# Kernel optimization log

Measured on AMD Instinct MI355X. Metric: run time of the kernel, lower is better.

Reference implementation:

```python
import jax, jax.numpy as jnp
import numpy as np
import math

B, NO, L = 128, 100, 36
VS, TS, D, H, NB = 2048, 1024, 1024, 8, 2
DH = D // H
SCALE = 1.0 / math.sqrt(DH)


def _shape(x):
    # [B, N, D] -> [B, H, N, DH]
    b, n, _ = x.shape
    return x.reshape(b, n, H, DH).transpose(0, 2, 1, 3)


def _unshape(x):
    # [B, H, N, DH] -> [B, N, D]
    return x.transpose(0, 2, 1, 3).reshape(x.shape[0], x.shape[2], D)


def _masked_softmax(scores, key_mask):
    # scores [B,H,Nq,Nk]; key_mask [B,Nk] float (1=valid, 0=pad)
    scores = jnp.where(key_mask[:, None, None, :] > 0, scores, -jnp.inf)
    return jax.nn.softmax(scores, axis=-1)


def _forward(v, t, vm, tm,
             vlin_w, vlin_b, tlin_w, tlin_b,
             iv_w, iv_b, it_w, it_b, ivo_w, ivo_b, ito_w, ito_b,
             gv_w, gv_b, gt_w, gt_b, av_w, av_b, at_w, at_b,
             avo_w, avo_b, ato_w, ato_b):
    # initial projection to hidden size (dropout is identity at drop=0.0)
    v = v @ vlin_w + vlin_b
    t = t @ tlin_w + tlin_b
    for _ in range(NB):  # weights shared across blocks (SingleBlock)
        # ---- InterModalityUpdate ----
        v = v * vm[..., None]
        t = t * tm[..., None]
        vt = jax.nn.relu(v) @ iv_w + iv_b   # [B,NO,3D]
        tt = jax.nn.relu(t) @ it_w + it_b   # [B,L,3D]
        vk, vq, vv = [_shape(a) for a in jnp.split(vt, 3, axis=2)]
        tk, tq, tv = [_shape(a) for a in jnp.split(tt, 3, axis=2)]
        t2v = _masked_softmax(jnp.einsum('bhnd,bhmd->bhnm', vq, tk) * SCALE, tm)
        v2t = _masked_softmax(jnp.einsum('bhnd,bhmd->bhnm', tq, vk) * SCALE, vm)
        v_up = _unshape(jnp.einsum('bhnm,bhmd->bhnd', t2v, tv))
        t_up = _unshape(jnp.einsum('bhnm,bhmd->bhnd', v2t, vv))
        v = jnp.concatenate([v, v_up], axis=2) @ ivo_w + ivo_b
        t = jnp.concatenate([t, t_up], axis=2) @ ito_w + ito_b
        # ---- DyIntraModalityUpdate ----
        v_mean = (v * vm[..., None]).sum(1) / vm.sum(1, keepdims=True)  # [B,D]
        t_mean = (t * tm[..., None]).sum(1) / tm.sum(1, keepdims=True)
        v4t_gate = jax.nn.sigmoid(jax.nn.relu(v_mean) @ gv_w + gv_b)  # gates text
        t4v_gate = jax.nn.sigmoid(jax.nn.relu(t_mean) @ gt_w + gt_b)  # gates vision
        gate_t = (1.0 + v4t_gate).reshape(-1, H, 1, DH)  # [B,H,1,DH]
        gate_v = (1.0 + t4v_gate).reshape(-1, H, 1, DH)
        vt2 = (jax.nn.relu(v) @ av_w + av_b) * vm[..., None]
        tt2 = (jax.nn.relu(t) @ at_w + at_b) * tm[..., None]
        vk2, vq2, vv2 = [_shape(a) for a in jnp.split(vt2, 3, axis=2)]
        tk2, tq2, tv2 = [_shape(a) for a in jnp.split(tt2, 3, axis=2)]
        v2v = _masked_softmax(jnp.einsum('bhnd,bhmd->bhnm', gate_v * vq2, gate_v * vk2) * SCALE, vm)
        t2t = _masked_softmax(jnp.einsum('bhnd,bhmd->bhnm', gate_t * tq2, gate_t * tk2) * SCALE, tm)
        v_up2 = _unshape(jnp.einsum('bhnm,bhmd->bhnd', v2v, vv2))
        t_up2 = _unshape(jnp.einsum('bhnm,bhmd->bhnd', t2t, tv2))
        v = (v + v_up2) @ avo_w + avo_b
        t = (t + t_up2) @ ato_w + ato_b
    return v, t


def setup_inputs() -> dict:
    key = jax.random.key(0)
    ks = list(jax.random.split(key, 20))
    WS = 0.02  # weight init scale

    def rn(k, shape, s=1.0):
        return jax.random.normal(k, shape, dtype=jnp.float32) * s

    inp = {
        'v': rn(ks[0], (B, NO, VS)),
        't': rn(ks[1], (B, L, TS)),
        'v_mask': jnp.ones((B, NO), dtype=jnp.float32),
        't_mask': jnp.ones((B, L), dtype=jnp.float32),
        'vlin_w': rn(ks[2], (VS, D), WS), 'vlin_b': jnp.zeros((D,), jnp.float32),
        'tlin_w': rn(ks[3], (TS, D), WS), 'tlin_b': jnp.zeros((D,), jnp.float32),
        'iv_w': rn(ks[4], (D, 3 * D), WS), 'iv_b': jnp.zeros((3 * D,), jnp.float32),
        'it_w': rn(ks[5], (D, 3 * D), WS), 'it_b': jnp.zeros((3 * D,), jnp.float32),
        'ivo_w': rn(ks[6], (2 * D, D), WS), 'ivo_b': jnp.zeros((D,), jnp.float32),
        'ito_w': rn(ks[7], (2 * D, D), WS), 'ito_b': jnp.zeros((D,), jnp.float32),
        'gv_w': rn(ks[8], (D, D), WS), 'gv_b': jnp.zeros((D,), jnp.float32),
        'gt_w': rn(ks[9], (D, D), WS), 'gt_b': jnp.zeros((D,), jnp.float32),
        'av_w': rn(ks[10], (D, 3 * D), WS), 'av_b': jnp.zeros((3 * D,), jnp.float32),
        'at_w': rn(ks[11], (D, 3 * D), WS), 'at_b': jnp.zeros((3 * D,), jnp.float32),
        'avo_w': rn(ks[12], (D, D), WS), 'avo_b': jnp.zeros((D,), jnp.float32),
        'ato_w': rn(ks[13], (D, D), WS), 'ato_b': jnp.zeros((D,), jnp.float32),
    }
    return inp


def reference(v, t, v_mask, t_mask,
              vlin_w, vlin_b, tlin_w, tlin_b,
              iv_w, iv_b, it_w, it_b, ivo_w, ivo_b, ito_w, ito_b,
              gv_w, gv_b, gt_w, gt_b, av_w, av_b, at_w, at_b,
              avo_w, avo_b, ato_w, ato_b):
    return _forward(v, t, v_mask, t_mask,
                    vlin_w, vlin_b, tlin_w, tlin_b,
                    iv_w, iv_b, it_w, it_b, ivo_w, ivo_b, ito_w, ito_b,
                    gv_w, gv_b, gt_w, gt_b, av_w, av_b, at_w, at_b,
                    avo_w, avo_b, ato_w, ato_b)
```

## Files before the change

### kernel.cpp

```cpp
#include <hip/hip_runtime.h>

typedef __bf16 bf16x8 __attribute__((ext_vector_type(8)));
typedef float f32x4 __attribute__((ext_vector_type(4)));

#define SCALEF 0.08838834764831843f
#define FL_SIG 2

__device__ __forceinline__ float bf2f(short u) {
    unsigned int x = ((unsigned int)(unsigned short)u) << 16;
    return __builtin_bit_cast(float, x);
}
__device__ __forceinline__ short f2bf(float f) {
    unsigned int x = __builtin_bit_cast(unsigned int, f);
    unsigned int r = (x + 0x7FFFu + ((x >> 16) & 1u)) >> 16;
    return (short)(unsigned short)r;
}
__device__ __forceinline__ unsigned int pkbf(float lo, float hi) {
    return ((unsigned int)(unsigned short)f2bf(lo)) | (((unsigned int)(unsigned short)f2bf(hi)) << 16);
}
__device__ __forceinline__ unsigned int relu_pk(unsigned int p) {
    unsigned int sgn = p & 0x80008000u;
    unsigned int m = (sgn >> 15) * 0xFFFFu;
    return p & ~m;
}
__device__ __forceinline__ void gload16(const void* g, void* l) {
    __builtin_amdgcn_global_load_lds(
        (const __attribute__((address_space(1))) unsigned int*)g,
        (__attribute__((address_space(3))) unsigned int*)l, 16, 0, 0);
}

struct GP {
    const short* A1; const short* A2; const short* WT;
    const float* bias; const float* rmask; void* C;
    int k2s, lda, M, N, K, ldc, flags;
};

template<int RELU, int CF32>
__global__ __launch_bounds__(256, 4) void gemm2_k(GP p0, GP p1)
{
    GP p = (blockIdx.z == 0) ? p0 : p1;
    const int nbx = p.N >> 7;
    const int nby = p.M >> 7;
    if ((int)blockIdx.y >= nby) return;

    __shared__ short lA[128 * 64];
    __shared__ short lB[128 * 64];
    const int tid = threadIdx.x;
    const int lane = tid & 63;
    const int wave = tid >> 6;
    const int wr = wave >> 1, wc = wave & 1;
    const int q16 = lane & 15, gk = lane >> 4;

    const int nwg = nbx * nby;
    int orig = blockIdx.y * nbx + blockIdx.x;
    int qq = nwg >> 3, rr = nwg & 7;
    int xcd = orig & 7, idx = orig >> 3;
    int swz = (xcd < rr ? xcd * (qq + 1) : rr * (qq + 1) + (xcd - rr) * qq) + idx;
    const int bn = (swz % nbx) * 128;
    const int bm = (swz / nbx) * 128;

    const int srow = lane >> 3;
    const int scol = ((lane & 7) ^ srow) * 8;

    f32x4 acc[4][4];
#pragma unroll
    for (int i = 0; i < 4; ++i)
#pragma unroll
        for (int j = 0; j < 4; ++j) acc[i][j] = (f32x4){0.f, 0.f, 0.f, 0.f};

    for (int k0 = 0; k0 < p.K; k0 += 64) {
        const short* Asrc = p.A1; int kc = k0;
        if (p.A2 != nullptr && k0 >= p.k2s) { Asrc = p.A2; kc = k0 - p.k2s; }
#pragma unroll
        for (int i = 0; i < 4; ++i) {
            int chunk = wave * 4 + i;
            int row = chunk * 8 + srow;
            gload16(Asrc + (size_t)(bm + row) * p.lda + kc + scol, lA + chunk * 512);
            gload16(p.WT + (size_t)(bn + row) * p.K + k0 + scol, lB + chunk * 512);
        }
        __syncthreads();
#pragma unroll
        for (int kk = 0; kk < 2; ++kk) {
            bf16x8 af[4], bfr[4];
#pragma unroll
            for (int i = 0; i < 4; ++i) {
                int row = wr * 64 + i * 16 + q16;
                int off = (row * 128 + kk * 64 + gk * 16) ^ ((row & 7) << 4);
                af[i] = *(const bf16x8*)((const char*)lA + off);
                if (RELU) {
                    union { bf16x8 v; unsigned int w[4]; } u;
                    u.v = af[i];
#pragma unroll
                    for (int t = 0; t < 4; ++t) u.w[t] = relu_pk(u.w[t]);
                    af[i] = u.v;
                }
            }
#pragma unroll
            for (int j = 0; j < 4; ++j) {
                int row = wc * 64 + j * 16 + q16;
                int off = (row * 128 + kk * 64 + gk * 16) ^ ((row & 7) << 4);
                bfr[j] = *(const bf16x8*)((const char*)lB + off);
            }
#pragma unroll
            for (int i = 0; i < 4; ++i)
#pragma unroll
                for (int j = 0; j < 4; ++j)
                    acc[i][j] = __builtin_amdgcn_mfma_f32_16x16x32_bf16(af[i], bfr[j], acc[i][j], 0, 0, 0);
        }
        __syncthreads();
    }
    const bool sig = (p.flags & FL_SIG) != 0;
#pragma unroll
    for (int i = 0; i < 4; ++i) {
#pragma unroll
        for (int j = 0; j < 4; ++j) {
            int col = bn + wc * 64 + j * 16 + q16;
            float bv = p.bias[col];
#pragma unroll
            for (int r = 0; r < 4; ++r) {
                int row = bm + wr * 64 + i * 16 + gk * 4 + r;
                float v = acc[i][j][r] + bv;
                if (sig) v = 1.f + 1.f / (1.f + __expf(-v));
                if (p.rmask) v *= p.rmask[row];
                if (CF32) ((float*)p.C)[(size_t)row * p.ldc + col] = v;
                else      ((short*)p.C)[(size_t)row * p.ldc + col] = f2bf(v);
            }
        }
    }
}

struct AP {
    const short* q; const short* kv; const float* mask; const short* gate;
    const short* add; short* out; int Nq, Nk;
};

__global__ __launch_bounds__(256, 2) void attn2_mfma(AP a0, AP a1)
{
    constexpr int KT = 7, KT2 = 4;
    constexpr int KROWS = KT * 16;
    constexpr int KV = KT2 * 32;
    constexpr int VROWB = KV * 2;
    __shared__ short sK[KROWS * 128];
    __shared__ short sVT[128 * KV];
    __shared__ float sMask[KV];

    AP a = (blockIdx.z == 0) ? a0 : a1;
    const int Nq = a.Nq, Nk = a.Nk;
    const int tid = threadIdx.x;
    const int h = blockIdx.x, b = blockIdx.y;
    const int lane = tid & 63, w = tid >> 6;
    const int g = lane >> 4, q16 = lane & 15;

    union U8 { uint4 u4; short s[8]; };

    for (int u = tid; u < Nk * 16; u += 256) {
        int k = u >> 4, seg = u & 15;
        U8 t; t.u4 = *(const uint4*)(a.kv + (size_t)(b * Nk + k) * 3072 + h * 128 + seg * 8);
        if (a.gate) {
            const short* gp = a.gate + b * 1024 + h * 128 + seg * 8;
#pragma unroll
            for (int j = 0; j < 8; ++j) {
                float gv = bf2f(gp[j]);
                t.s[j] = f2bf(bf2f(t.s[j]) * gv * gv);
            }
        }
        int off = (k * 256 + seg * 16) ^ ((k & 7) << 4);
        *(uint4*)((char*)sK + off) = t.u4;
    }
    for (int u = tid; u < Nk * 16; u += 256) {
        int k = u >> 4, seg = u & 15;
        U8 t; t.u4 = *(const uint4*)(a.kv + (size_t)(b * Nk + k) * 3072 + 2048 + h * 128 + seg * 8);
#pragma unroll
        for (int j = 0; j < 8; ++j) {
            int d = seg * 8 + j;
            int off = (d * VROWB + ((k >> 3) << 4) + (k & 7) * 2) ^ ((d & 7) << 4);
            *(short*)((char*)sVT + off) = t.s[j];
        }
    }
    for (int u = tid; u < (KV - Nk) * 128; u += 256) {
        int k = Nk + (u >> 7), d = u & 127;
        int off = (d * VROWB + ((k >> 3) << 4) + (k & 7) * 2) ^ ((d & 7) << 4);
        *(short*)((char*)sVT + off) = 0;
    }
    for (int u = tid; u < KV; u += 256)
        sMask[u] = (u < Nk) ? a.mask[b * Nk + u] : 0.f;
    __syncthreads();

    const int QT = (Nq + 15) >> 4;
    for (int qt = w; qt < QT; qt += 4) {
        int qrow = qt * 16 + q16; if (qrow >= Nq) qrow = Nq - 1;
        const short* qp = a.q + (size_t)(b * Nq + qrow) * 3072 + 1024 + h * 128 + g * 8;
        bf16x8 qf[4];
#pragma unroll
        for (int ks = 0; ks < 4; ++ks)
            qf[ks] = *(const bf16x8*)(qp + ks * 32);

        f32x4 accs[KT];
#pragma unroll
        for (int kt = 0; kt < KT; ++kt) accs[kt] = (f32x4){0.f, 0.f, 0.f, 0.f};
#pragma unroll
        for (int kt = 0; kt < KT; ++kt) {
            int krow = kt * 16 + q16;
#pragma unroll
            for (int ks = 0; ks < 4; ++ks) {
                bf16x8 kf = *(const bf16x8*)((char*)sK +
                    ((krow * 256 + ks * 64 + g * 16) ^ ((krow & 7) << 4)));
                accs[kt] = __builtin_amdgcn_mfma_f32_16x16x32_bf16(kf, qf[ks], accs[kt], 0, 0, 0);
            }
        }
        float pv[KT][4];
        float mx = -__builtin_inff();
#pragma unroll
        for (int kt = 0; kt < KT; ++kt)
#pragma unroll
            for (int r = 0; r < 4; ++r) {
                int k = kt * 16 + g * 4 + r;
                float s = (sMask[k] > 0.f) ? accs[kt][r] * SCALEF : -__builtin_inff();
                pv[kt][r] = s;
                mx = fmaxf(mx, s);
            }
        mx = fmaxf(mx, __shfl_xor(mx, 16, 64));
        mx = fmaxf(mx, __shfl_xor(mx, 32, 64));
        float sum = 0.f;
#pragma unroll
        for (int kt = 0; kt < KT; ++kt)
#pragma unroll
            for (int r = 0; r < 4; ++r) {
                float p = __expf(pv[kt][r] - mx);
                pv[kt][r] = p;
                sum += p;
            }
        sum += __shfl_xor(sum, 16, 64);
        sum += __shfl_xor(sum, 32, 64);
        float rden = 1.f / sum;

        unsigned int wA[KT2 * 2], wB[KT2 * 2];
#pragma unroll
        for (int t = 0; t < KT2 * 2; ++t) {
            if (t < KT) { wA[t] = pkbf(pv[t][0], pv[t][1]); wB[t] = pkbf(pv[t][2], pv[t][3]); }
            else { wA[t] = 0u; wB[t] = 0u; }
        }
        f32x4 acco[8];
#pragma unroll
        for (int dt = 0; dt < 8; ++dt) acco[dt] = (f32x4){0.f, 0.f, 0.f, 0.f};
        const int srcA = (((g & 1) * 2) * 16 + q16) * 4;
        const int srcB = (((g & 1) * 2 + 1) * 16 + q16) * 4;
        const bool hi = g >= 2;
#pragma unroll
        for (int kt2 = 0; kt2 < KT2; ++kt2) {
            int a0_ = __builtin_amdgcn_ds_bpermute(srcA, (int)wA[2 * kt2]);
            int a1_ = __builtin_amdgcn_ds_bpermute(srcA, (int)wA[2 * kt2 + 1]);
            int b0_ = __builtin_amdgcn_ds_bpermute(srcA, (int)wB[2 * kt2]);
            int b1_ = __builtin_amdgcn_ds_bpermute(srcA, (int)wB[2 * kt2 + 1]);
            int c0_ = __builtin_amdgcn_ds_bpermute(srcB, (int)wA[2 * kt2]);
            int c1_ = __builtin_amdgcn_ds_bpermute(srcB, (int)wA[2 * kt2 + 1]);
            int d0_ = __builtin_amdgcn_ds_bpermute(srcB, (int)wB[2 * kt2]);
            int d1_ = __builtin_amdgcn_ds_bpermute(srcB, (int)wB[2 * kt2 + 1]);
            union { int wd[4]; bf16x8 v; } pf;
            pf.wd[0] = hi ? a1_ : a0_;
            pf.wd[1] = hi ? b1_ : b0_;
            pf.wd[2] = hi ? c1_ : c0_;
            pf.wd[3] = hi ? d1_ : d0_;
#pragma unroll
            for (int dt = 0; dt < 8; ++dt) {
                int drow = dt * 16 + q16;
                bf16x8 vf = *(const bf16x8*)((char*)sVT +
                    ((drow * VROWB + kt2 * 64 + g * 16) ^ ((drow & 7) << 4)));
                acco[dt] = __builtin_amdgcn_mfma_f32_16x16x32_bf16(pf.v, vf, acco[dt], 0, 0, 0);
            }
        }
        float rd[4];
#pragma unroll
        for (int r = 0; r < 4; ++r) {
            int rv = __builtin_amdgcn_ds_bpermute((g * 4 + r) * 4, __builtin_bit_cast(int, rden));
            rd[r] = __builtin_bit_cast(float, rv);
        }
#pragma unroll
        for (int dt = 0; dt < 8; ++dt)
#pragma unroll
            for (int r = 0; r < 4; ++r) {
                int q = qt * 16 + g * 4 + r;
                if (q < Nq) {
                    size_t oidx = (size_t)(b * Nq + q) * 1024 + h * 128 + dt * 16 + q16;
                    float val = acco[dt][r] * rd[r];
                    if (a.add) val += bf2f(a.add[oidx]);
                    a.out[oidx] = f2bf(val);
                }
            }
    }
}

struct TP { const float* W; short* WT; int K, N, nblk; };
struct TPack { TP t[12]; };

__global__ void transpose12_k(TPack pk) {
    __shared__ short tile[32][33];
    int bid = blockIdx.x;
    int pi = 0;
    while (bid >= pk.t[pi].nblk) { bid -= pk.t[pi].nblk; ++pi; }
    const float* W = pk.t[pi].W;
    short* WT = pk.t[pi].WT;
    int K = pk.t[pi].K, N = pk.t[pi].N;
    int nbx = N >> 5;
    int nb = (bid % nbx) * 32, kb = (bid / nbx) * 32;
    int tx = threadIdx.x & 31, ty = threadIdx.x >> 5;
    for (int i = ty; i < 32; i += 8)
        tile[i][tx] = f2bf(W[(size_t)(kb + i) * N + nb + tx]);
    __syncthreads();
    for (int i = ty; i < 32; i += 8)
        WT[(size_t)(nb + i) * K + kb + tx] = tile[tx][i];
}

__global__ void cvt2_bf(const float* __restrict__ a, short* __restrict__ oa, int na8,
                        const float* __restrict__ b, short* __restrict__ ob, int nb8) {
    int i = blockIdx.x * 256 + threadIdx.x;
    const float* src; short* dst; int loc;
    if (i < na8) { src = a; dst = oa; loc = i; }
    else if (i < na8 + nb8) { src = b; dst = ob; loc = i - na8; }
    else return;
    const float4* p = (const float4*)(src + (size_t)loc * 8);
    float4 x = p[0], y = p[1];
    uint4 val;
    val.x = pkbf(x.x, x.y); val.y = pkbf(x.z, x.w);
    val.z = pkbf(y.x, y.y); val.w = pkbf(y.z, y.w);
    *(uint4*)(dst + (size_t)loc * 8) = val;
}

__global__ void mean2_k(const short* __restrict__ Xv, const float* __restrict__ mv, short* __restrict__ ov_,
                        const short* __restrict__ Xt, const float* __restrict__ mt, short* __restrict__ ot_) {
    int idx = blockIdx.x * 256 + threadIdx.x;
    const short* X; const float* mk; short* o; int N; int loc;
    if (idx < 131072) { X = Xv; mk = mv; o = ov_; N = 100; loc = idx; }
    else { X = Xt; mk = mt; o = ot_; N = 36; loc = idx - 131072; }
    int b = loc >> 10, d = loc & 1023;
    float s = 0.f, c = 0.f;
    for (int n = 0; n < N; ++n) {
        float m = mk[b * N + n];
        s += bf2f(X[(size_t)(b * N + n) * 1024 + d]) * m;
        c += m;
    }
    o[loc] = f2bf(s / c);
}

extern "C" void kernel_launch(void* const* d_in, const int* in_sizes, int n_in,
                              void* d_out, int out_size, void* d_ws, size_t ws_size,
                              hipStream_t stream)
{
    const float* v_in  = (const float*)d_in[0];
    const float* t_in  = (const float*)d_in[1];
    const float* vm    = (const float*)d_in[2];
    const float* tm    = (const float*)d_in[3];
    const float* vlin_w = (const float*)d_in[4];  const float* vlin_b = (const float*)d_in[5];
    const float* tlin_w = (const float*)d_in[6];  const float* tlin_b = (const float*)d_in[7];
    const float* iv_w  = (const float*)d_in[8];   const float* iv_b  = (const float*)d_in[9];
    const float* it_w  = (const float*)d_in[10];  const float* it_b  = (const float*)d_in[11];
    const float* ivo_w = (const float*)d_in[12];  const float* ivo_b = (const float*)d_in[13];
    const float* ito_w = (const float*)d_in[14];  const float* ito_b = (const float*)d_in[15];
    const float* gv_w  = (const float*)d_in[16];  const float* gv_b  = (const float*)d_in[17];
    const float* gt_w  = (const float*)d_in[18];  const float* gt_b  = (const float*)d_in[19];
    const float* av_w  = (const float*)d_in[20];  const float* av_b  = (const float*)d_in[21];
    const float* at_w  = (const float*)d_in[22];  const float* at_b  = (const float*)d_in[23];
    const float* avo_w = (const float*)d_in[24];  const float* avo_b = (const float*)d_in[25];
    const float* ato_w = (const float*)d_in[26];  const float* ato_b = (const float*)d_in[27];

    short* ws = (short*)d_ws;
    const size_t WTvlin = 0;
    const size_t WTtlin = 2097152;
    const size_t WTiv   = 3145728;
    const size_t WTit   = 6291456;
    const size_t WTivo  = 9437184;
    const size_t WTito  = 11534336;
    const size_t WTgv   = 13631488;
    const size_t WTgt   = 14680064;
    const size_t WTav   = 15728640;
    const size_t WTat   = 18874368;
    const size_t WTavo  = 22020096;
    const size_t WTato  = 23068672;
    const size_t V_A    = 24117248;
    const size_t V_B    = 37224448;
    const size_t T_A    = 50331648;
    const size_t T_B    = 55050240;
    const size_t VT     = 59768832;
    const size_t TT     = 99090432;
    const size_t V_UP   = 113246208;
    const size_t T_UP   = 126353408;
    const size_t VMEAN  = 131072000;
    const size_t TMEAN  = 131203072;
    const size_t GATEV  = 131334144;
    const size_t GATET  = 131465216;
    const size_t TOTAL  = 131596288;
    if (ws_size < TOTAL * 2ull) return;

    short* v_a = ws + V_A; short* v_b = ws + V_B;
    short* t_a = ws + T_A; short* t_b = ws + T_B;
    short* vt = ws + VT;   short* tt = ws + TT;
    short* v_up = ws + V_UP; short* t_up = ws + T_UP;
    short* vmean = ws + VMEAN; short* tmean = ws + TMEAN;
    short* gateV = ws + GATEV; short* gateT = ws + GATET;
    float* ov = (float*)d_out;
    float* ot = ov + 13107200;

    {
        TPack pk;
        auto set = [&](int i, const float* W, size_t off, int K, int N) {
            pk.t[i] = TP{W, ws + off, K, N, (N / 32) * (K / 32)};
        };
        set(0, vlin_w, WTvlin, 2048, 1024);  set(1, tlin_w, WTtlin, 1024, 1024);
        set(2, iv_w, WTiv, 1024, 3072);      set(3, it_w, WTit, 1024, 3072);
        set(4, ivo_w, WTivo, 2048, 1024);    set(5, ito_w, WTito, 2048, 1024);
        set(6, gv_w, WTgv, 1024, 1024);      set(7, gt_w, WTgt, 1024, 1024);
        set(8, av_w, WTav, 1024, 3072);      set(9, at_w, WTat, 1024, 3072);
        set(10, avo_w, WTavo, 1024, 1024);   set(11, ato_w, WTato, 1024, 1024);
        int total = 0;
        for (int i = 0; i < 12; ++i) total += pk.t[i].nblk;
        transpose12_k<<<total, 256, 0, stream>>>(pk);
    }

    auto GPm = [&](const short* A1, const short* A2, int k2s, int lda, size_t WToff,
                   const float* bp, const float* rm, void* Cp, int M, int N, int K, int flags) {
        return GP{A1, A2, ws + WToff, bp, rm, Cp, k2s, lda, M, N, K, N, flags};
    };
    auto APm = [&](const short* q, const short* kv, const float* mk, const short* gt,
                   const short* adds, short* o, int Nq, int Nk) {
        return AP{q, kv, mk, gt, adds, o, Nq, Nk};
    };

    {
        short* v_cv = ws + VT;
        short* t_cv = ws + TT;
        int na8 = 12800 * 2048 / 8, nb8 = 4608 * 1024 / 8;
        cvt2_bf<<<(na8 + nb8 + 255) / 256, 256, 0, stream>>>(v_in, v_cv, na8, t_in, t_cv, nb8);
        gemm2_k<0, 0><<<dim3(8, 100, 2), 256, 0, stream>>>(
            GPm(v_cv, nullptr, 0, 2048, WTvlin, vlin_b, vm, v_a, 12800, 1024, 2048, 0),
            GPm(t_cv, nullptr, 0, 1024, WTtlin, tlin_b, tm, t_a, 4608, 1024, 1024, 0));
    }

    for (int ib = 0; ib < 2; ++ib) {
        gemm2_k<1, 0><<<dim3(24, 100, 2), 256, 0, stream>>>(
            GPm(v_a, nullptr, 0, 1024, WTiv, iv_b, nullptr, vt, 12800, 3072, 1024, 0),
            GPm(t_a, nullptr, 0, 1024, WTit, it_b, nullptr, tt, 4608, 3072, 1024, 0));
        attn2_mfma<<<dim3(8, 128, 2), 256, 0, stream>>>(
            APm(vt, tt, tm, nullptr, nullptr, v_up, 100, 36),
            APm(tt, vt, vm, nullptr, nullptr, t_up, 36, 100));
        gemm2_k<0, 0><<<dim3(8, 100, 2), 256, 0, stream>>>(
            GPm(v_a, v_up, 1024, 1024, WTivo, ivo_b, nullptr, v_b, 12800, 1024, 2048, 0),
            GPm(t_a, t_up, 1024, 1024, WTito, ito_b, nullptr, t_b, 4608, 1024, 2048, 0));
        mean2_k<<<1024, 256, 0, stream>>>(v_b, vm, vmean, t_b, tm, tmean);
        gemm2_k<1, 0><<<dim3(8, 1, 2), 256, 0, stream>>>(
            GPm(vmean, nullptr, 0, 1024, WTgv, gv_b, nullptr, gateT, 128, 1024, 1024, FL_SIG),
            GPm(tmean, nullptr, 0, 1024, WTgt, gt_b, nullptr, gateV, 128, 1024, 1024, FL_SIG));
        gemm2_k<1, 0><<<dim3(24, 100, 2), 256, 0, stream>>>(
            GPm(v_b, nullptr, 0, 1024, WTav, av_b, vm, vt, 12800, 3072, 1024, 0),
            GPm(t_b, nullptr, 0, 1024, WTat, at_b, tm, tt, 4608, 3072, 1024, 0));
        attn2_mfma<<<dim3(8, 128, 2), 256, 0, stream>>>(
            APm(vt, vt, vm, gateV, v_b, v_up, 100, 100),
            APm(tt, tt, tm, gateT, t_b, t_up, 36, 36));
        if (ib == 1) {
            gemm2_k<0, 1><<<dim3(8, 100, 2), 256, 0, stream>>>(
                GPm(v_up, nullptr, 0, 1024, WTavo, avo_b, nullptr, ov, 12800, 1024, 1024, 0),
                GPm(t_up, nullptr, 0, 1024, WTato, ato_b, nullptr, ot, 4608, 1024, 1024, 0));
        } else {
            gemm2_k<0, 0><<<dim3(8, 100, 2), 256, 0, stream>>>(
                GPm(v_up, nullptr, 0, 1024, WTavo, avo_b, vm, v_a, 12800, 1024, 1024, 0),
                GPm(t_up, nullptr, 0, 1024, WTato, ato_b, tm, t_a, 4608, 1024, 1024, 0));
        }
    }
}
```

Baseline: 1.702 ms.

## Add 256x256 triple-buffered GEMM for QKV projections and specialize attention key tiles

```diff
diff --git a/kernel.cpp b/kernel.cpp
--- a/kernel.cpp
+++ b/kernel.cpp
@@ -34,6 +34,120 @@
     const float* bias; const float* rmask; void* C;
     int k2s, lda, M, N, K, ldc, flags;
 };
+
+template<int RELU>
+__global__ __launch_bounds__(512, 2) void gemm3_k(GP p0, GP p1)
+{
+    GP p = (blockIdx.z == 0) ? p0 : p1;
+    const int nbx = p.N >> 8;
+    const int nby = p.M >> 8;
+    if ((int)blockIdx.y >= nby) return;
+
+    __shared__ short lA[3 * 8192];
+    __shared__ short lB[3 * 8192];
+    const int tid = threadIdx.x;
+    const int lane = tid & 63;
+    const int wave = tid >> 6;
+    const int wr = wave >> 2, wc = wave & 3;
+    const int q16 = lane & 15, gk = lane >> 4;
+
+    const int nwg = nbx * nby;
+    int orig = blockIdx.y * nbx + blockIdx.x;
+    int qq = nwg >> 3, rr = nwg & 7;
+    int xcd = orig & 7, idx = orig >> 3;
+    int swz = (xcd < rr ? xcd * (qq + 1) : rr * (qq + 1) + (xcd - rr) * qq) + idx;
+    const int bn = (swz % nbx) * 256;
+    const int bm = (swz / nbx) * 256;
+
+    const int NT = p.K >> 5;
+
+    f32x4 acc[8][4];
+#pragma unroll
+    for (int i = 0; i < 8; ++i)
+#pragma unroll
+        for (int j = 0; j < 4; ++j) acc[i][j] = (f32x4){0.f, 0.f, 0.f, 0.f};
+
+    const int strow0 = tid >> 2;
+    const int sslot = tid & 3;
+
+    auto STAGE3 = [&](int t) {
+        int buf = t % 3;
+        int kc = t << 5;
+#pragma unroll
+        for (int issue = 0; issue < 2; ++issue) {
+            int row = issue * 128 + strow0;
+            int h = (row + (row >> 2)) & 3;
+            int gcol = ((sslot ^ h) << 3);
+            short* dstA = lA + buf * 8192 + issue * 4096 + wave * 512;
+            short* dstB = lB + buf * 8192 + issue * 4096 + wave * 512;
+            gload16(p.A1 + (size_t)(bm + row) * p.lda + kc + gcol, dstA);
+            gload16(p.WT + (size_t)(bn + row) * p.K + kc + gcol, dstB);
+        }
+    };
+
+    STAGE3(0);
+    STAGE3(1);
+    asm volatile("s_waitcnt vmcnt(4)" ::: "memory");
+    __builtin_amdgcn_s_barrier();
+
+    for (int j = 0; j < NT; ++j) {
+        int buf = j % 3;
+        if (j + 2 < NT) STAGE3(j + 2);
+
+        bf16x8 af[8], bfr[4];
+#pragma unroll
+        for (int i = 0; i < 8; ++i) {
+            int ra = wr * 128 + i * 16 + q16;
+            int off = buf * 8192 + ra * 32 + ((gk ^ ((ra + (ra >> 2)) & 3)) << 3);
+            af[i] = *(const bf16x8*)(lA + off);
+            if (RELU) {
+                union { bf16x8 v; unsigned int w[4]; } u;
+                u.v = af[i];
+#pragma unroll
+                for (int t2 = 0; t2 < 4; ++t2) u.w[t2] = relu_pk(u.w[t2]);
+                af[i] = u.v;
+            }
+        }
+#pragma unroll
+        for (int jj = 0; jj < 4; ++jj) {
+            int rb = wc * 64 + jj * 16 + q16;
+            int off = buf * 8192 + rb * 32 + ((gk ^ ((rb + (rb >> 2)) & 3)) << 3);
+            bfr[jj] = *(const bf16x8*)(lB + off);
+        }
+        __builtin_amdgcn_s_setprio(1);
+#pragma unroll
+        for (int i = 0; i < 8; ++i)
+#pragma unroll
+            for (int jj = 0; jj < 4; ++jj)
+                acc[i][jj] = __builtin_amdgcn_mfma_f32_16x16x32_bf16(af[i], bfr[jj], acc[i][jj], 0, 0, 0);
+        __builtin_amdgcn_s_setprio(0);
+
+        if (j + 2 < NT) {
+            asm volatile("s_waitcnt vmcnt(4)" ::: "memory");
+        } else if (j + 1 < NT) {
+            asm volatile("s_waitcnt vmcnt(0)" ::: "memory");
+        }
+        __builtin_amdgcn_s_barrier();
+    }
+
+    const bool sig = (p.flags & FL_SIG) != 0;
+#pragma unroll
+    for (int i = 0; i < 8; ++i) {
+#pragma unroll
+        for (int jj = 0; jj < 4; ++jj) {
+            int col = bn + wc * 64 + jj * 16 + q16;
+            float bv = p.bias[col];
+#pragma unroll
+            for (int r = 0; r < 4; ++r) {
+                int row = bm + wr * 128 + i * 16 + gk * 4 + r;
+                float v = acc[i][jj][r] + bv;
+                if (sig) v = 1.f + 1.f / (1.f + __expf(-v));
+                if (p.rmask) v *= p.rmask[row];
+                ((short*)p.C)[(size_t)row * p.ldc + col] = f2bf(v);
+            }
+        }
+    }
+}
 
 template<int RELU, int CF32>
 __global__ __launch_bounds__(256, 4) void gemm2_k(GP p0, GP p1)
@@ -134,17 +248,12 @@
     const short* add; short* out; int Nq, Nk;
 };
 
-__global__ __launch_bounds__(256, 2) void attn2_mfma(AP a0, AP a1)
+template<int KT>
+__device__ __forceinline__ void attn_body(const AP& a, short* sK, short* sVT, float* sMask)
 {
-    constexpr int KT = 7, KT2 = 4;
-    constexpr int KROWS = KT * 16;
+    constexpr int KT2 = (KT + 1) / 2;
     constexpr int KV = KT2 * 32;
     constexpr int VROWB = KV * 2;
-    __shared__ short sK[KROWS * 128];
-    __shared__ short sVT[128 * KV];
-    __shared__ float sMask[KV];
-
-    AP a = (blockIdx.z == 0) ? a0 : a1;
     const int Nq = a.Nq, Nk = a.Nk;
     const int tid = threadIdx.x;
     const int h = blockIdx.x, b = blockIdx.y;
@@ -226,9 +335,9 @@
         for (int kt = 0; kt < KT; ++kt)
 #pragma unroll
             for (int r = 0; r < 4; ++r) {
-                float p = __expf(pv[kt][r] - mx);
-                pv[kt][r] = p;
-                sum += p;
+                float pp = __expf(pv[kt][r] - mx);
+                pv[kt][r] = pp;
+                sum += pp;
             }
         sum += __shfl_xor(sum, 16, 64);
         sum += __shfl_xor(sum, 32, 64);
@@ -288,6 +397,16 @@
                 }
             }
     }
+}
+
+template<int KT0, int KT1>
+__global__ __launch_bounds__(256, 2) void attn2_mfma(AP a0, AP a1)
+{
+    __shared__ short sK[112 * 128];
+    __shared__ short sVT[128 * 128];
+    __shared__ float sMask[128];
+    if (blockIdx.z == 0) attn_body<KT0>(a0, sK, sVT, sMask);
+    else                 attn_body<KT1>(a1, sK, sVT, sMask);
 }
 
 struct TP { const float* W; short* WT; int K, N, nblk; };
@@ -436,10 +555,10 @@
     }
 
     for (int ib = 0; ib < 2; ++ib) {
-        gemm2_k<1, 0><<<dim3(24, 100, 2), 256, 0, stream>>>(
+        gemm3_k<1><<<dim3(12, 50, 2), 512, 0, stream>>>(
             GPm(v_a, nullptr, 0, 1024, WTiv, iv_b, nullptr, vt, 12800, 3072, 1024, 0),
             GPm(t_a, nullptr, 0, 1024, WTit, it_b, nullptr, tt, 4608, 3072, 1024, 0));
-        attn2_mfma<<<dim3(8, 128, 2), 256, 0, stream>>>(
+        attn2_mfma<3, 7><<<dim3(8, 128, 2), 256, 0, stream>>>(
             APm(vt, tt, tm, nullptr, nullptr, v_up, 100, 36),
             APm(tt, vt, vm, nullptr, nullptr, t_up, 36, 100));
         gemm2_k<0, 0><<<dim3(8, 100, 2), 256, 0, stream>>>(
@@ -449,10 +568,10 @@
         gemm2_k<1, 0><<<dim3(8, 1, 2), 256, 0, stream>>>(
             GPm(vmean, nullptr, 0, 1024, WTgv, gv_b, nullptr, gateT, 128, 1024, 1024, FL_SIG),
             GPm(tmean, nullptr, 0, 1024, WTgt, gt_b, nullptr, gateV, 128, 1024, 1024, FL_SIG));
-        gemm2_k<1, 0><<<dim3(24, 100, 2), 256, 0, stream>>>(
+        gemm3_k<1><<<dim3(12, 50, 2), 512, 0, stream>>>(
             GPm(v_b, nullptr, 0, 1024, WTav, av_b, vm, vt, 12800, 3072, 1024, 0),
             GPm(t_b, nullptr, 0, 1024, WTat, at_b, tm, tt, 4608, 3072, 1024, 0));
-        attn2_mfma<<<dim3(8, 128, 2), 256, 0, stream>>>(
+        attn2_mfma<7, 3><<<dim3(8, 128, 2), 256, 0, stream>>>(
             APm(vt, vt, vm, gateV, v_b, v_up, 100, 100),
             APm(tt, tt, tm, gateT, t_b, t_up, 36, 36));
         if (ib == 1) {
```

Measured after the change: 2.038 ms. 19.7% more time.
